# Kernel optimization log

Hardware: AMD Instinct MI355X
Metric: run time of the kernel (lower is better)

## Reference

```python
import jax, jax.numpy as jnp
import numpy as np

EPS = 1e-7
CAPS_N = 1152   # 32 maps * 6 * 6
CAPS1_DIM = 8
CAPS2_N = 10
CAPS2_DIM = 16


def squash(s, axis):
    sq = jnp.sum(jnp.square(s), axis=axis, keepdims=True)
    norm = jnp.sqrt(sq + EPS)
    return (sq / (1.0 + sq)) * (s / norm)


def _conv(x, k, b, stride):
    y = jax.lax.conv_general_dilated(x, k, (stride, stride), 'VALID',
                                     dimension_numbers=('NHWC', 'HWIO', 'NHWC'))
    return jax.nn.relu(y + b)


def setup_inputs() -> dict:
    key = jax.random.key(0)
    ks = jax.random.split(key, 8)
    B = 256
    return {
        'image': jax.random.uniform(ks[0], (B, 28, 28, 1), dtype=jnp.float32),
        'target': jax.random.randint(ks[1], (B,), 0, CAPS2_N),
        'conv1_w': jax.random.normal(ks[2], (9, 9, 1, 256), jnp.float32) * 0.05,
        'conv1_b': jnp.zeros((256,), jnp.float32),
        'conv2_w': jax.random.normal(ks[3], (9, 9, 256, 256), jnp.float32) * 0.02,
        'conv2_b': jnp.zeros((256,), jnp.float32),
        'W': jax.random.normal(ks[4], (1, CAPS_N, CAPS2_N, CAPS2_DIM, CAPS1_DIM), jnp.float32) * 0.1,
        'd1_w': jax.random.normal(ks[5], (CAPS2_N * CAPS2_DIM, 512), jnp.float32) * 0.05,
        'd1_b': jnp.zeros((512,), jnp.float32),
        'd2_w': jax.random.normal(ks[6], (512, 1024), jnp.float32) * 0.04,
        'd2_b': jnp.zeros((1024,), jnp.float32),
        'd3_w': jax.random.normal(ks[7], (1024, 784), jnp.float32) * 0.03,
        'd3_b': jnp.zeros((784,), jnp.float32),
    }


def reference(image, target, conv1_w, conv1_b, conv2_w, conv2_b, W,
              d1_w, d1_b, d2_w, d2_b, d3_w, d3_b):
    B = image.shape[0]
    h = _conv(image, conv1_w, conv1_b, 1)        # [B,20,20,256]
    h = _conv(h, conv2_w, conv2_b, 2)            # [B,6,6,256]
    pc = squash(h.reshape(B, CAPS_N, CAPS1_DIM), axis=-1)  # [B,1152,8]
    # u_hat[b,n,c,j] = sum_i W[0,n,c,j,i] * pc[b,n,i]  (avoids explicit tiling)
    u_hat = jnp.einsum('ncji,bni->bncj', W[0], pc)          # [B,1152,10,16]
    # round 1: softmax of zeros over the 10 digit caps == uniform 1/10
    s1 = jnp.sum(u_hat, axis=1) * (1.0 / CAPS2_N)           # [B,10,16]
    v1 = squash(s1, axis=-1)
    # agreement uv[b,n,c] = <u_hat[b,n,c,:], v1[b,c,:]>
    uv = jnp.einsum('bncj,bcj->bnc', u_hat, v1)             # [B,1152,10]
    # round 2
    c2 = jax.nn.softmax(uv, axis=2)
    s2 = jnp.einsum('bnc,bncj->bcj', c2, u_hat)             # [B,10,16]
    v2 = squash(s2, axis=-1)                                # [B,10,16]
    norm_v2 = jnp.sqrt(jnp.sum(jnp.square(v2), axis=-1, keepdims=True) + EPS)
    norm_v2 = norm_v2[:, None, :, :, None]                  # [B,1,10,1,1]
    y_pred = jnp.squeeze(jnp.argmax(norm_v2, axis=2), axis=(1, 2))  # [B,1]
    # training path: mask by target one-hot
    mask = jax.nn.one_hot(target, CAPS2_N, dtype=v2.dtype)  # [B,10]
    masked = v2 * mask[:, :, None]                          # [B,10,16]
    flat = masked.reshape(B, 1, CAPS2_N * CAPS2_DIM)        # [B,1,160]
    h1 = jax.nn.relu(flat @ d1_w + d1_b)
    h2 = jax.nn.relu(h1 @ d2_w + d2_b)
    dec = jax.nn.sigmoid(h2 @ d3_w + d3_b)                  # [B,1,784]
    return norm_v2, y_pred, dec
```

## Files before the change

kernel.cpp:

```cpp
#include <hip/hip_runtime.h>
#include <math.h>

#define EPS 1e-7f
#define IN1_ELEMS 26214400
#define BT_ELEMS  5308416

typedef float fvec4 __attribute__((ext_vector_type(4)));
typedef short short8 __attribute__((ext_vector_type(8)));
typedef _Float16 half8 __attribute__((ext_vector_type(8)));

__device__ inline unsigned short f2h(float f){
  _Float16 h = (_Float16)f;
  return __builtin_bit_cast(unsigned short, h);
}
__device__ inline float h2f(unsigned short u){
  return (float)__builtin_bit_cast(_Float16, u);
}
__device__ inline void async16(unsigned short* dst, const unsigned short* src){
  __builtin_amdgcn_global_load_lds((const __attribute__((address_space(1))) void*)src,
                                   (__attribute__((address_space(3))) void*)dst, 16, 0, 0);
}
__device__ inline fvec4 mfma_f16(short8 a, short8 b, fvec4 c){
  return __builtin_amdgcn_mfma_f32_16x16x32_f16(
      __builtin_bit_cast(half8, a), __builtin_bit_cast(half8, b), c, 0, 0, 0);
}

__global__ __launch_bounds__(256) void prep_kernel(const float* __restrict__ w2,
    unsigned short* __restrict__ BTh, unsigned short* __restrict__ BTl,
    float* __restrict__ c2out,
    const float* __restrict__ img, const float* __restrict__ w1,
    const float* __restrict__ b1, unsigned short* __restrict__ outh,
    float* __restrict__ s1s2){
  const int bid = blockIdx.x;
  const int t = threadIdx.x;
  if (bid < 1296){
    __shared__ float tile[64][65];
    int k0 = (bid % 324) * 64, oc0 = (bid / 324) * 64;
    for (int g = bid*256 + t; g < 2359296; g += 1296*256) c2out[g] = 0.f;
    #pragma unroll
    for (int p = 0; p < 16; ++p){
      int f = p*256 + t;
      int kr = f >> 6, cc = f & 63;
      tile[kr][cc] = w2[(size_t)(k0 + kr)*256 + oc0 + cc];
    }
    __syncthreads();
    #pragma unroll
    for (int p = 0; p < 16; ++p){
      int f = p*256 + t;
      int ocr = f >> 6, kc = f & 63;
      float v = tile[kc][ocr] * 64.f;
      unsigned short h = f2h(v);
      size_t idx = (size_t)(oc0 + ocr)*20736 + k0 + kc;
      BTh[idx] = h;
      BTl[idx] = f2h(v - h2f(h));
    }
  } else {
    const int cid = bid - 1296;
    if (cid < 320) s1s2[cid*256 + t] = 0.f;
    __shared__ float sim[252];
    int oh = cid % 20, b = cid / 20;
    if (t < 252) sim[t] = img[((size_t)b*28 + oh + t/28)*28 + (t%28)];
    __syncthreads();
    float acc[20];
    #pragma unroll
    for (int i = 0; i < 20; ++i) acc[i] = 0.f;
    #pragma unroll
    for (int kh = 0; kh < 9; ++kh){
      float im[28];
      #pragma unroll
      for (int c = 0; c < 28; ++c) im[c] = sim[kh*28 + c];
      #pragma unroll
      for (int kw = 0; kw < 9; ++kw){
        float wv = w1[(kh*9 + kw)*256 + t];
        #pragma unroll
        for (int ow = 0; ow < 20; ++ow) acc[ow] = fmaf(im[ow + kw], wv, acc[ow]);
      }
    }
    float bv = b1[t];
    size_t base = ((size_t)(b*20 + oh))*20*256 + t;
    #pragma unroll
    for (int ow = 0; ow < 20; ++ow){
      float v = fmaxf(acc[ow] + bv, 0.f);
      outh[base + ow*256] = f2h(v * 0.015625f);
    }
  }
}

__global__ __launch_bounds__(256) void conv2_mfma(const unsigned short* __restrict__ in1h,
    const unsigned short* __restrict__ BTh, float* __restrict__ out){
  __shared__ __align__(16) unsigned short lds[24576];
  const int t = threadIdx.x;
  const int lane = t & 63, w = t >> 6;
  const int m0 = blockIdx.y * 128, n0 = blockIdx.x * 128;
  const int rowA = t >> 2, q = (t & 3) ^ ((t >> 3) & 3);

  const unsigned short* aS[2];
  const unsigned short* bS[2];
  #pragma unroll
  for (int h = 0; h < 2; ++h){
    int m = m0 + h*64 + rowA;
    int bb = m / 36, s = m - bb*36, oh = s / 6, ow = s - oh*6;
    aS[h] = in1h + ((size_t)((bb*20 + 2*oh)*20 + 2*ow))*256 + q*8;
    int n = n0 + h*64 + rowA;
    bS[h] = BTh + (size_t)n*20736 + q*8;
  }

  const int r = lane & 15;
  const int p = (lane >> 4) ^ ((lane >> 1) & 3);
  int roA[4], roB[4];
  #pragma unroll
  for (int i=0;i<4;++i){
    roA[i] = ((w >> 1)*64 + i*16 + r)*32 + p*8;
    roB[i] = ((w & 1)*64  + i*16 + r)*32 + p*8;
  }

  fvec4 acc[4][4];
  #pragma unroll
  for (int i=0;i<4;++i)
    #pragma unroll
    for (int j=0;j<4;++j) acc[i][j] = (fvec4){0.f,0.f,0.f,0.f};

  const int ks0 = blockIdx.z * 81;

  #define STAGE(BUF, KS) do{                                            \
    int kk_ = (KS) >> 3, kh_ = kk_/9, kw_ = kk_ - kh_*9;                \
    int aoff_ = (kh_*20 + kw_)*256 + ((KS) & 7)*32;                     \
    int boff_ = (KS)*32;                                                \
    int base_ = (BUF)*12288;                                            \
    _Pragma("unroll")                                                   \
    for (int h_=0; h_<2; ++h_){                                         \
      async16(&lds[base_ +        h_*2048 + t*8], aS[h_] + aoff_);      \
      async16(&lds[base_ + 4096 + h_*2048 + t*8], bS[h_] + boff_);      \
      async16(&lds[base_ + 8192 + h_*2048 + t*8], bS[h_] + BT_ELEMS + boff_); \
    } }while(0)

  STAGE(0, ks0);
  int buf = 0;
  for (int it = 0; it < 81; ++it){
    __syncthreads();
    if (it < 80) STAGE(buf^1, ks0 + it + 1);
    int base = buf*12288;
    short8 af[4], bh[4], bl[4];
    #pragma unroll
    for (int i=0;i<4;++i){
      af[i] = *(const short8*)&lds[base + roA[i]];
      bh[i] = *(const short8*)&lds[base + 4096 + roB[i]];
      bl[i] = *(const short8*)&lds[base + 8192 + roB[i]];
    }
    #pragma unroll
    for (int i=0;i<4;++i)
      #pragma unroll
      for (int j=0;j<4;++j){
        acc[i][j] = mfma_f16(af[i], bh[j], acc[i][j]);
        acc[i][j] = mfma_f16(af[i], bl[j], acc[i][j]);
      }
    buf ^= 1;
  }

  const int qm = (w >> 1)*64, qn = (w & 1)*64;
  #pragma unroll
  for (int i=0;i<4;++i){
    int gm = m0 + qm + i*16 + ((lane >> 4) << 2);
    #pragma unroll
    for (int j=0;j<4;++j){
      int gn = n0 + qn + j*16 + (lane & 15);
      #pragma unroll
      for (int rr=0;rr<4;++rr)
        atomicAdd(&out[(size_t)(gm + rr)*256 + gn], acc[i][j][rr]);
    }
  }
}

__global__ __launch_bounds__(256) void s1pc_kernel(const float* __restrict__ c2out,
    const float* __restrict__ b2, float* __restrict__ pc,
    const float* __restrict__ Wm, float* __restrict__ s1){
  __shared__ float pcl[2048];
  int t = threadIdx.x;
  int n0 = blockIdx.x * 16, b0 = blockIdx.y * 16;
  int pix = n0 >> 5, oc0 = (n0 & 31) * 8;
  {
    int bl = t >> 4, part = t & 15;
    const float* s = c2out + ((size_t)((b0 + bl)*36 + pix))*256 + oc0 + part*8;
    float v[8], sq = 0.f;
    #pragma unroll
    for (int e=0;e<8;++e){
      float x = fmaxf(s[e] + b2[oc0 + part*8 + e], 0.f);
      v[e] = x; sq += x*x;
    }
    float fac = sq / ((1.f + sq) * sqrtf(sq + EPS));
    float* o = pc + ((size_t)(b0 + bl)*1152 + n0 + part)*8;
    float* l = &pcl[(bl*16 + part)*8];
    #pragma unroll
    for (int e=0;e<8;++e){ float y = v[e]*fac; o[e] = y; l[e] = y; }
  }
  __syncthreads();
  for (int r = 0; r < 10; ++r){
    int item = r*256 + t;
    int bl = item / 160, cj = item - bl*160;
    float s1a = 0.f;
    const float* pb = &pcl[bl*128];
    #pragma unroll 4
    for (int nl = 0; nl < 16; ++nl){
      const float4* wp = (const float4*)&Wm[((size_t)(n0 + nl)*160 + cj)*8];
      float4 w0 = wp[0], w1 = wp[1];
      const float4* pp = (const float4*)&pb[nl*8];
      float4 p0 = pp[0], p1 = pp[1];
      s1a += w0.x*p0.x + w0.y*p0.y + w0.z*p0.z + w0.w*p0.w
           + w1.x*p1.x + w1.y*p1.y + w1.z*p1.z + w1.w*p1.w;
    }
    atomicAdd(&s1[(b0 + bl)*160 + cj], s1a);
  }
}

__global__ __launch_bounds__(320) void routing2(const float* __restrict__ pc,
    const float* __restrict__ Wm, const float* __restrict__ s1, float* __restrict__ s2){
  __shared__ float pcl[32][128];
  __shared__ float v1l[16][160];
  __shared__ float facl[160];
  __shared__ float c2l[32][10][16];
  const int t = threadIdx.x;
  const int n0 = blockIdx.x*32, b0 = blockIdx.y*16;

  for (int f = t; f < 4096; f += 320){
    int nl = f >> 7, rem = f & 127;
    pcl[nl][rem] = pc[((size_t)(b0 + (rem >> 3))*1152 + n0 + nl)*8 + (rem & 7)];
  }
  if (t < 160){
    int b = t/10, c = t - (t/10)*10;
    const float* s = s1 + (size_t)(b0 + b)*160 + c*16;
    float sq = 0.f;
    #pragma unroll
    for (int j=0;j<16;++j){ float v = s[j]*0.1f; sq += v*v; }
    facl[t] = 0.1f * sq / ((1.f + sq) * sqrtf(sq + EPS));
  }
  __syncthreads();
  for (int f = t; f < 2560; f += 320){
    int b = f / 160, cj = f - b*160;
    v1l[b][cj] = s1[(size_t)(b0 + b)*160 + cj] * facl[b*10 + (cj >> 4)];
  }
  __syncthreads();

  {
    const int nl = t / 10, c = t - (t/10)*10;
    const float* wrow = Wm + ((size_t)(n0 + nl)*160 + c*16)*8;
    #pragma unroll
    for (int g = 0; g < 2; ++g){
      float pcr[64];
      #pragma unroll
      for (int u = 0; u < 16; ++u)
        ((float4*)pcr)[u] = ((const float4*)&pcl[nl][g*64])[u];
      float uv[8];
      #pragma unroll
      for (int b=0;b<8;++b) uv[b] = 0.f;
      #pragma unroll
      for (int j = 0; j < 16; ++j){
        float4 w0 = ((const float4*)wrow)[j*2], w1 = ((const float4*)wrow)[j*2+1];
        #pragma unroll
        for (int b=0;b<8;++b){
          float tj = w0.x*pcr[b*8+0] + w0.y*pcr[b*8+1] + w0.z*pcr[b*8+2] + w0.w*pcr[b*8+3]
                   + w1.x*pcr[b*8+4] + w1.y*pcr[b*8+5] + w1.z*pcr[b*8+6] + w1.w*pcr[b*8+7];
          uv[b] = fmaf(tj, v1l[g*8+b][c*16 + j], uv[b]);
        }
      }
      #pragma unroll
      for (int b=0;b<8;++b) c2l[nl][c][g*8+b] = uv[b];
    }
  }
  __syncthreads();

  for (int idx = t; idx < 512; idx += 320){
    int snl = idx >> 4, sb = idx & 15;
    float mx = c2l[snl][0][sb];
    #pragma unroll
    for (int cc=1;cc<10;++cc) mx = fmaxf(mx, c2l[snl][cc][sb]);
    float e[10], sum = 0.f;
    #pragma unroll
    for (int cc=0;cc<10;++cc){ e[cc] = expf(c2l[snl][cc][sb] - mx); sum += e[cc]; }
    float inv = 1.f/sum;
    #pragma unroll
    for (int cc=0;cc<10;++cc) c2l[snl][cc][sb] = e[cc]*inv;
  }
  __syncthreads();

  {
    const int g = t / 160, cj = t - (t/160)*160;
    const int c = cj >> 4;
    float acc[16];
    #pragma unroll
    for (int b=0;b<16;++b) acc[b] = 0.f;
    for (int nn = 0; nn < 16; ++nn){
      int nl = g*16 + nn;
      const float4* wp = (const float4*)&Wm[((size_t)(n0 + nl)*160 + cj)*8];
      float4 w0 = wp[0], w1 = wp[1];
      #pragma unroll
      for (int b=0;b<16;++b){
        const float4* pp = (const float4*)&pcl[nl][b*8];
        float4 p0 = pp[0], p1 = pp[1];
        float uh = w0.x*p0.x + w0.y*p0.y + w0.z*p0.z + w0.w*p0.w
                 + w1.x*p1.x + w1.y*p1.y + w1.z*p1.z + w1.w*p1.w;
        acc[b] = fmaf(c2l[nl][c][b], uh, acc[b]);
      }
    }
    #pragma unroll
    for (int b=0;b<16;++b)
      atomicAdd(&s2[(size_t)(b0 + b)*160 + cj], acc[b]);
  }
}

__global__ __launch_bounds__(128) void final_dec1(const float* __restrict__ s2,
    const int* __restrict__ target, const float* __restrict__ d1w,
    const float* __restrict__ d1b, float* __restrict__ out_norm,
    float* __restrict__ out_pred, float* __restrict__ h1){
  __shared__ float v2t[16];
  __shared__ float nrm[10];
  int b = blockIdx.x, t = threadIdx.x;
  int tg = target[b];
  if (t < 10){
    const float* s = s2 + b*160 + t*16;
    float x[16], sq = 0.f;
    #pragma unroll
    for (int j=0;j<16;++j){ x[j] = s[j]; sq += x[j]*x[j]; }
    float fac = sq / ((1.f + sq) * sqrtf(sq + EPS));
    float n2 = 0.f;
    #pragma unroll
    for (int j=0;j<16;++j){
      float v = x[j]*fac;
      if (t == tg) v2t[j] = v;
      n2 += v*v;
    }
    float nr = sqrtf(n2 + EPS);
    nrm[t] = nr;
    out_norm[b*10 + t] = nr;
  }
  __syncthreads();
  if (t == 0){
    int am = 0; float bv = nrm[0];
    #pragma unroll
    for (int c=1;c<10;++c) if (nrm[c] > bv){ bv = nrm[c]; am = c; }
    out_pred[b] = (float)am;
  }
  float v[16];
  #pragma unroll
  for (int j=0;j<16;++j) v[j] = v2t[j];
  #pragma unroll
  for (int rr = 0; rr < 4; ++rr){
    int n = t + rr*128;
    float acc = d1b[n];
    #pragma unroll
    for (int j=0;j<16;++j) acc = fmaf(v[j], d1w[(size_t)(tg*16 + j)*512 + n], acc);
    h1[(size_t)b*512 + n] = fmaxf(acc, 0.f);
  }
}

__global__ __launch_bounds__(256) void dec_gemm(const float* __restrict__ A,
    const float* __restrict__ B, const float* __restrict__ bias, float* __restrict__ C,
    int K, int N, int act){
  int t = threadIdx.x;
  int n = blockIdx.x*64 + (t & 63);
  int m = blockIdx.y*4 + (t >> 6);
  if (n >= N) return;
  float acc = 0.f;
  const float* a = A + (size_t)m*K;
  const float* bp = B + n;
  #pragma unroll 8
  for (int k = 0; k < K; ++k) acc = fmaf(a[k], bp[(size_t)k*N], acc);
  acc += bias[n];
  if (act == 0) acc = fmaxf(acc, 0.f);
  else acc = 1.f/(1.f + expf(-acc));
  C[(size_t)m*N + n] = acc;
}

extern "C" void kernel_launch(void* const* d_in, const int* in_sizes, int n_in,
                              void* d_out, int out_size, void* d_ws, size_t ws_size,
                              hipStream_t stream) {
  const float* image   = (const float*)d_in[0];
  const int*   target  = (const int*)d_in[1];
  const float* conv1_w = (const float*)d_in[2];
  const float* conv1_b = (const float*)d_in[3];
  const float* conv2_w = (const float*)d_in[4];
  const float* conv2_b = (const float*)d_in[5];
  const float* Wm      = (const float*)d_in[6];
  const float* d1_w    = (const float*)d_in[7];
  const float* d1_b    = (const float*)d_in[8];
  const float* d2_w    = (const float*)d_in[9];
  const float* d2_b    = (const float*)d_in[10];
  const float* d3_w    = (const float*)d_in[11];
  const float* d3_b    = (const float*)d_in[12];

  char* ws = (char*)d_ws;
  unsigned short* in1h = (unsigned short*)(ws);
  unsigned short* BTh  = (unsigned short*)(ws + 52428800);
  float* c2out  = (float*)(ws + 73662464);
  float* pc     = (float*)(ws + 83099648);
  float* s1     = (float*)(ws + 92536832);
  float* s2     = (float*)(ws + 92700672);
  float* h1     = (float*)(ws + 92864512);
  float* h2     = (float*)(ws + 93388800);

  float* out_norm = (float*)d_out;
  float* out_pred = out_norm + 2560;
  float* dec      = out_norm + 2816;

  prep_kernel<<<dim3(6416),256,0,stream>>>(conv2_w, BTh, BTh + BT_ELEMS, c2out,
                                           image, conv1_w, conv1_b, in1h, s1);
  conv2_mfma<<<dim3(2,72,8),256,0,stream>>>(in1h, BTh, c2out);
  s1pc_kernel<<<dim3(72,16),256,0,stream>>>(c2out, conv2_b, pc, Wm, s1);
  routing2<<<dim3(36,16),320,0,stream>>>(pc, Wm, s1, s2);
  final_dec1<<<dim3(256),128,0,stream>>>(s2, target, d1_w, d1_b, out_norm, out_pred, h1);
  dec_gemm<<<dim3(16,64),256,0,stream>>>(h1, d2_w, d2_b, h2, 512, 1024, 0);
  dec_gemm<<<dim3(13,64),256,0,stream>>>(h2, d3_w, d3_b, dec, 1024, 784, 1);
}
```

Before: 690.0 us.

## Cache u_hat in shared memory in routing2 and register-block decoder GEMM rows

routing2 now computes u_hat once per block into shared memory and reuses it for both the agreement and the weighted-sum passes, instead of recomputing it twice from W and pc. Blocks are shrunk to 8 capsules by 8 batch rows, so the grid grows from 36x16 to 144x32. That raises parallelism but also multiplies W reloads across batch tiles and the atomic adds into s2. Separately, dec_gemm now computes 4 output rows per thread, so each B-matrix load is reused across those rows, and the grid is reduced accordingly.

Result: faster. 656.3 us (-4.9%).

```diff
diff --git a/kernel.cpp b/kernel.cpp
--- a/kernel.cpp
+++ b/kernel.cpp
@@ -214,18 +214,19 @@
 
 __global__ __launch_bounds__(320) void routing2(const float* __restrict__ pc,
     const float* __restrict__ Wm, const float* __restrict__ s1, float* __restrict__ s2){
-  __shared__ float pcl[32][128];
-  __shared__ float v1l[16][160];
-  __shared__ float facl[160];
-  __shared__ float c2l[32][10][16];
+  __shared__ float pcl[8][64];
+  __shared__ float v1l[8][160];
+  __shared__ float facl[80];
+  __shared__ float uhl[8][160][8];
+  __shared__ float c2l[8][10][8];
   const int t = threadIdx.x;
-  const int n0 = blockIdx.x*32, b0 = blockIdx.y*16;
-
-  for (int f = t; f < 4096; f += 320){
-    int nl = f >> 7, rem = f & 127;
+  const int n0 = blockIdx.x*8, b0 = blockIdx.y*8;
+
+  for (int f = t; f < 512; f += 320){
+    int nl = f >> 6, rem = f & 63;
     pcl[nl][rem] = pc[((size_t)(b0 + (rem >> 3))*1152 + n0 + nl)*8 + (rem & 7)];
   }
-  if (t < 160){
+  if (t < 80){
     int b = t/10, c = t - (t/10)*10;
     const float* s = s1 + (size_t)(b0 + b)*160 + c*16;
     float sq = 0.f;
@@ -234,42 +235,45 @@
     facl[t] = 0.1f * sq / ((1.f + sq) * sqrtf(sq + EPS));
   }
   __syncthreads();
-  for (int f = t; f < 2560; f += 320){
+  for (int f = t; f < 1280; f += 320){
     int b = f / 160, cj = f - b*160;
     v1l[b][cj] = s1[(size_t)(b0 + b)*160 + cj] * facl[b*10 + (cj >> 4)];
   }
+
+  #pragma unroll
+  for (int rr = 0; rr < 4; ++rr){
+    int idx = rr*320 + t;
+    int nl = idx / 160, cj = idx - nl*160;
+    const float4* wp = (const float4*)&Wm[((size_t)(n0 + nl)*160 + cj)*8];
+    float4 w0 = wp[0], w1 = wp[1];
+    #pragma unroll
+    for (int b = 0; b < 8; ++b){
+      const float4* pp = (const float4*)&pcl[nl][b*8];
+      float4 p0 = pp[0], p1 = pp[1];
+      uhl[nl][cj][b] = w0.x*p0.x + w0.y*p0.y + w0.z*p0.z + w0.w*p0.w
+                     + w1.x*p1.x + w1.y*p1.y + w1.z*p1.z + w1.w*p1.w;
+    }
+  }
   __syncthreads();
 
   {
-    const int nl = t / 10, c = t - (t/10)*10;
-    const float* wrow = Wm + ((size_t)(n0 + nl)*160 + c*16)*8;
-    #pragma unroll
-    for (int g = 0; g < 2; ++g){
-      float pcr[64];
-      #pragma unroll
-      for (int u = 0; u < 16; ++u)
-        ((float4*)pcr)[u] = ((const float4*)&pcl[nl][g*64])[u];
-      float uv[8];
-      #pragma unroll
-      for (int b=0;b<8;++b) uv[b] = 0.f;
-      #pragma unroll
-      for (int j = 0; j < 16; ++j){
-        float4 w0 = ((const float4*)wrow)[j*2], w1 = ((const float4*)wrow)[j*2+1];
-        #pragma unroll
-        for (int b=0;b<8;++b){
-          float tj = w0.x*pcr[b*8+0] + w0.y*pcr[b*8+1] + w0.z*pcr[b*8+2] + w0.w*pcr[b*8+3]
-                   + w1.x*pcr[b*8+4] + w1.y*pcr[b*8+5] + w1.z*pcr[b*8+6] + w1.w*pcr[b*8+7];
-          uv[b] = fmaf(tj, v1l[g*8+b][c*16 + j], uv[b]);
-        }
-      }
-      #pragma unroll
-      for (int b=0;b<8;++b) c2l[nl][c][g*8+b] = uv[b];
-    }
-  }
-  __syncthreads();
-
-  for (int idx = t; idx < 512; idx += 320){
-    int snl = idx >> 4, sb = idx & 15;
+    const int nl = t / 40, rest = t - (t/40)*40;
+    const int c = rest >> 2, b2 = (rest & 3)*2;
+    float uv0 = 0.f, uv1 = 0.f;
+    #pragma unroll
+    for (int j = 0; j < 16; ++j){
+      const float* up = &uhl[nl][c*16 + j][b2];
+      float vj0 = v1l[b2][c*16 + j], vj1 = v1l[b2+1][c*16 + j];
+      uv0 = fmaf(up[0], vj0, uv0);
+      uv1 = fmaf(up[1], vj1, uv1);
+    }
+    c2l[nl][c][b2]   = uv0;
+    c2l[nl][c][b2+1] = uv1;
+  }
+  __syncthreads();
+
+  if (t < 64){
+    int snl = t >> 3, sb = t & 7;
     float mx = c2l[snl][0][sb];
     #pragma unroll
     for (int cc=1;cc<10;++cc) mx = fmaxf(mx, c2l[snl][cc][sb]);
@@ -285,25 +289,20 @@
   {
     const int g = t / 160, cj = t - (t/160)*160;
     const int c = cj >> 4;
-    float acc[16];
-    #pragma unroll
-    for (int b=0;b<16;++b) acc[b] = 0.f;
-    for (int nn = 0; nn < 16; ++nn){
-      int nl = g*16 + nn;
-      const float4* wp = (const float4*)&Wm[((size_t)(n0 + nl)*160 + cj)*8];
-      float4 w0 = wp[0], w1 = wp[1];
-      #pragma unroll
-      for (int b=0;b<16;++b){
-        const float4* pp = (const float4*)&pcl[nl][b*8];
-        float4 p0 = pp[0], p1 = pp[1];
-        float uh = w0.x*p0.x + w0.y*p0.y + w0.z*p0.z + w0.w*p0.w
-                 + w1.x*p1.x + w1.y*p1.y + w1.z*p1.z + w1.w*p1.w;
-        acc[b] = fmaf(c2l[nl][c][b], uh, acc[b]);
-      }
-    }
-    #pragma unroll
-    for (int b=0;b<16;++b)
-      atomicAdd(&s2[(size_t)(b0 + b)*160 + cj], acc[b]);
+    float acc0 = 0.f, acc1 = 0.f, acc2 = 0.f, acc3 = 0.f;
+    #pragma unroll
+    for (int nl = 0; nl < 8; ++nl){
+      const float4 uh = *(const float4*)&uhl[nl][cj][g*4];
+      const float4 cc = *(const float4*)&c2l[nl][c][g*4];
+      acc0 = fmaf(cc.x, uh.x, acc0);
+      acc1 = fmaf(cc.y, uh.y, acc1);
+      acc2 = fmaf(cc.z, uh.z, acc2);
+      acc3 = fmaf(cc.w, uh.w, acc3);
+    }
+    atomicAdd(&s2[(size_t)(b0 + g*4 + 0)*160 + cj], acc0);
+    atomicAdd(&s2[(size_t)(b0 + g*4 + 1)*160 + cj], acc1);
+    atomicAdd(&s2[(size_t)(b0 + g*4 + 2)*160 + cj], acc2);
+    atomicAdd(&s2[(size_t)(b0 + g*4 + 3)*160 + cj], acc3);
   }
 }
 
@@ -357,17 +356,35 @@
     int K, int N, int act){
   int t = threadIdx.x;
   int n = blockIdx.x*64 + (t & 63);
-  int m = blockIdx.y*4 + (t >> 6);
+  int m0 = blockIdx.y*16 + (t >> 6)*4;
   if (n >= N) return;
-  float acc = 0.f;
-  const float* a = A + (size_t)m*K;
+  float acc0 = 0.f, acc1 = 0.f, acc2 = 0.f, acc3 = 0.f;
+  const float* a0 = A + (size_t)m0*K;
+  const float* a1 = a0 + K;
+  const float* a2 = a1 + K;
+  const float* a3 = a2 + K;
   const float* bp = B + n;
-  #pragma unroll 8
-  for (int k = 0; k < K; ++k) acc = fmaf(a[k], bp[(size_t)k*N], acc);
-  acc += bias[n];
-  if (act == 0) acc = fmaxf(acc, 0.f);
-  else acc = 1.f/(1.f + expf(-acc));
-  C[(size_t)m*N + n] = acc;
+  #pragma unroll 4
+  for (int k = 0; k < K; ++k){
+    float bv = bp[(size_t)k*N];
+    acc0 = fmaf(a0[k], bv, acc0);
+    acc1 = fmaf(a1[k], bv, acc1);
+    acc2 = fmaf(a2[k], bv, acc2);
+    acc3 = fmaf(a3[k], bv, acc3);
+  }
+  float bb = bias[n];
+  acc0 += bb; acc1 += bb; acc2 += bb; acc3 += bb;
+  if (act == 0){
+    acc0 = fmaxf(acc0, 0.f); acc1 = fmaxf(acc1, 0.f);
+    acc2 = fmaxf(acc2, 0.f); acc3 = fmaxf(acc3, 0.f);
+  } else {
+    acc0 = 1.f/(1.f + expf(-acc0)); acc1 = 1.f/(1.f + expf(-acc1));
+    acc2 = 1.f/(1.f + expf(-acc2)); acc3 = 1.f/(1.f + expf(-acc3));
+  }
+  C[(size_t)m0*N + n] = acc0;
+  C[(size_t)(m0+1)*N + n] = acc1;
+  C[(size_t)(m0+2)*N + n] = acc2;
+  C[(size_t)(m0+3)*N + n] = acc3;
 }
 
 extern "C" void kernel_launch(void* const* d_in, const int* in_sizes, int n_in,
@@ -405,8 +422,8 @@
                                            image, conv1_w, conv1_b, in1h, s1);
   conv2_mfma<<<dim3(2,72,8),256,0,stream>>>(in1h, BTh, c2out);
   s1pc_kernel<<<dim3(72,16),256,0,stream>>>(c2out, conv2_b, pc, Wm, s1);
-  routing2<<<dim3(36,16),320,0,stream>>>(pc, Wm, s1, s2);
+  routing2<<<dim3(144,32),320,0,stream>>>(pc, Wm, s1, s2);
   final_dec1<<<dim3(256),128,0,stream>>>(s2, target, d1_w, d1_b, out_norm, out_pred, h1);
-  dec_gemm<<<dim3(16,64),256,0,stream>>>(h1, d2_w, d2_b, h2, 512, 1024, 0);
-  dec_gemm<<<dim3(13,64),256,0,stream>>>(h2, d3_w, d3_b, dec, 1024, 784, 1);
-}
+  dec_gemm<<<dim3(16,16),256,0,stream>>>(h1, d2_w, d2_b, h2, 512, 1024, 0);
+  dec_gemm<<<dim3(13,16),256,0,stream>>>(h2, d3_w, d3_b, dec, 1024, 784, 1);
+}
```
